# Performance work log

Measured on AMD Instinct MI355X. Metric: run time of the kernel, lower is better.

Reference implementation:

```python
import jax, jax.numpy as jnp
import numpy as np

NUM_EXPERTS = 8
TOP_K = 2
HIDDEN = 2048
INTER = 2048
SWIGLU_LIMIT = 7.0
BATCH, SEQ = 4, 2048


def setup_inputs() -> dict:
    key = jax.random.key(0)
    k0, k1, k2, k3, k4 = jax.random.split(key, 5)
    x = jax.random.normal(k0, (BATCH, SEQ, HIDDEN), jnp.float32)
    Wr = jax.random.normal(k1, (HIDDEN, NUM_EXPERTS), jnp.float32) * 0.02
    Wg = jax.random.normal(k2, (NUM_EXPERTS, HIDDEN, INTER), jnp.float32) * 0.02
    Wu = jax.random.normal(k3, (NUM_EXPERTS, HIDDEN, INTER), jnp.float32) * 0.02
    Wd = jax.random.normal(k4, (NUM_EXPERTS, INTER, HIDDEN), jnp.float32) * 0.02
    return {"hidden_states": x, "Wr": Wr, "Wg": Wg, "Wu": Wu, "Wd": Wd}


def reference(hidden_states, Wr, Wg, Wu, Wd):
    # Router: logits [B,S,E], top-k over experts, softmax over the k logits.
    router_logits = jnp.einsum('bsh,he->bse', hidden_states, Wr)
    topk_logits, selected = jax.lax.top_k(router_logits, TOP_K)  # [B,S,K]
    router_probs = jax.nn.softmax(topk_logits, axis=-1)          # [B,S,K]

    # Per-expert masked-dense SwiGLU. Because the Dense layers have no bias,
    # Expert(x * mask) == Expert(x) at selected positions and the combine
    # weight is 0 elsewhere, so running on unmasked x is mathematically
    # identical to the original's masked-input formulation.
    out = jnp.zeros_like(hidden_states)
    for e in range(NUM_EXPERTS):  # fixed structural loop over experts
        w_e = jnp.where(selected == e, router_probs, 0.0).sum(axis=-1, keepdims=True)  # [B,S,1]
        g = jnp.einsum('bsh,hi->bsi', hidden_states, Wg[e])
        g = jnp.clip(jax.nn.silu(g), -SWIGLU_LIMIT, SWIGLU_LIMIT)
        u = jnp.einsum('bsh,hi->bsi', hidden_states, Wu[e])
        h = jnp.einsum('bsi,ih->bsh', g * u, Wd[e])
        out = out + h * w_e
    return out
```

## Files before the change

### kernel.cpp

```cpp
#include <hip/hip_runtime.h>

#define TOKENS 8192
#define HID 2048
#define NEXP 8
#define NT 32

typedef float f32x4 __attribute__((ext_vector_type(4)));
typedef short bf16x8 __attribute__((ext_vector_type(8)));

#define WS_XBF     0ULL
#define WS_ACT     33554432ULL
#define WS_WCAT    100663296ULL
#define WS_WDT     234881024ULL
#define WS_ROWTOK  301989888ULL
#define WS_ROWPROB 302055424ULL
#define WS_EIDX    302120960ULL
#define WS_PROBS   302186496ULL
#define WS_META    302252032ULL

__device__ __forceinline__ unsigned short f2bf(float f) {
    union { float f; unsigned int u; } a; a.f = f;
    unsigned int r = a.u + 0x7fffu + ((a.u >> 16) & 1u);
    return (unsigned short)(r >> 16);
}

__device__ __forceinline__ void gload16(void* ldsdst, const void* gsrc) {
    __builtin_amdgcn_global_load_lds(
        (const __attribute__((address_space(1))) void*)gsrc,
        (__attribute__((address_space(3))) void*)ldsdst, 16, 0, 0);
}

#define BAR asm volatile("s_barrier" ::: "memory")
#define VM4 asm volatile("s_waitcnt vmcnt(4)" ::: "memory")
#define VM0 asm volatile("s_waitcnt vmcnt(0)" ::: "memory")

__global__ __launch_bounds__(256) void router_kernel(
    const float* __restrict__ x, const float* __restrict__ Wr,
    unsigned short* __restrict__ xbf, int2* __restrict__ eidx,
    float2* __restrict__ probs, int* __restrict__ meta) {
    __shared__ float wrt[NEXP * HID];
    int tid = threadIdx.x;
    for (int f = tid; f < HID * NEXP; f += 256) {
        int i = f >> 3, e = f & 7;
        wrt[e * HID + i] = Wr[f];
    }
    __syncthreads();
    int w = tid >> 6, l = tid & 63;
    int tok = blockIdx.x * 4 + w;
    const float4* xr = (const float4*)(x + (size_t)tok * HID);
    float acc[NEXP];
#pragma unroll
    for (int e = 0; e < NEXP; ++e) acc[e] = 0.f;
    unsigned long long* xbr = (unsigned long long*)(xbf + (size_t)tok * HID);
#pragma unroll
    for (int it = 0; it < 8; ++it) {
        float4 v = xr[it * 64 + l];
        int k0 = (it * 64 + l) * 4;
#pragma unroll
        for (int e = 0; e < NEXP; ++e) {
            float4 wv = *(const float4*)&wrt[e * HID + k0];
            acc[e] += v.x * wv.x + v.y * wv.y + v.z * wv.z + v.w * wv.w;
        }
        unsigned long long pk = (unsigned long long)f2bf(v.x)
                              | ((unsigned long long)f2bf(v.y) << 16)
                              | ((unsigned long long)f2bf(v.z) << 32)
                              | ((unsigned long long)f2bf(v.w) << 48);
        int qi = ((k0 >> 5) << 3) + (((k0 >> 2) & 3) << 1) + ((k0 >> 4) & 1);
        xbr[qi] = pk;
    }
#pragma unroll
    for (int e = 0; e < NEXP; ++e) {
#pragma unroll
        for (int d = 1; d < 64; d <<= 1) acc[e] += __shfl_xor(acc[e], d, 64);
    }
    if (l == 0) {
        int e0 = 0; float v0 = acc[0];
#pragma unroll
        for (int e = 1; e < NEXP; ++e) if (acc[e] > v0) { v0 = acc[e]; e0 = e; }
        int e1 = -1; float v1 = 0.f;
#pragma unroll
        for (int e = 0; e < NEXP; ++e)
            if (e != e0 && (e1 < 0 || acc[e] > v1)) { v1 = acc[e]; e1 = e; }
        float a = __expf(v1 - v0);
        float inv = 1.f / (1.f + a);
        int2 ei; ei.x = e0; ei.y = e1;
        float2 pp; pp.x = inv; pp.y = a * inv;
        eidx[tok] = ei;
        probs[tok] = pp;
        atomicAdd(&meta[e0], 1);
        atomicAdd(&meta[e1], 1);
    }
}

__global__ __launch_bounds__(256) void convert_kernel(
    const float* __restrict__ Wg, const float* __restrict__ Wu,
    const float* __restrict__ Wd, unsigned short* __restrict__ wcat,
    unsigned short* __restrict__ wdt) {
    int mz = blockIdx.z;
    int mat = mz >> 3, e = mz & 7;
    const float* W = (mat == 0 ? Wg : (mat == 1 ? Wu : Wd)) + (size_t)e * HID * HID;
    int kb = blockIdx.y * 64, nb = blockIdx.x * 64;
    __shared__ unsigned short t[64][68];
    int tid = threadIdx.x;
    int kr = tid >> 4;
    int nc = (tid & 15) * 4;
#pragma unroll
    for (int ki = 0; ki < 4; ++ki) {
        int k = kr + ki * 16;
        float4 v = *(const float4*)&W[(size_t)(kb + k) * HID + nb + nc];
        t[nc + 0][k] = f2bf(v.x);
        t[nc + 1][k] = f2bf(v.y);
        t[nc + 2][k] = f2bf(v.z);
        t[nc + 3][k] = f2bf(v.w);
    }
    __syncthreads();
    int q = tid & 15;
    int k0 = ((q >> 3) << 5) + (((q >> 1) & 3) << 2) + ((q & 1) << 4);
#pragma unroll
    for (int ni = 0; ni < 4; ++ni) {
        int n = (tid >> 4) + ni * 16;
        int gn = nb + n;
        unsigned short* orow;
        if (mat < 2)
            orow = wcat + ((size_t)e * 4096 + (gn >> 4) * 32 + mat * 16 + (gn & 15)) * HID;
        else
            orow = wdt + ((size_t)e * HID + gn) * HID;
        unsigned long long pk = (unsigned long long)t[n][k0]
                              | ((unsigned long long)t[n][k0 + 1] << 16)
                              | ((unsigned long long)t[n][k0 + 2] << 32)
                              | ((unsigned long long)t[n][k0 + 3] << 48);
        *(unsigned long long*)&orow[kb + q * 4] = pk;
    }
}

__global__ void scan_kernel(int* __restrict__ meta) {
    if (threadIdx.x == 0) {
        int s = 0;
#pragma unroll
        for (int e = 0; e < NEXP; ++e) { meta[16 + e] = s; s += meta[e]; }
    }
}

__global__ __launch_bounds__(256) void build_kernel(
    const int2* __restrict__ eidx, const float2* __restrict__ probs,
    int* __restrict__ meta, int* __restrict__ row_token, float* __restrict__ row_prob) {
    int t = blockIdx.x * 256 + threadIdx.x;
    if (t >= TOKENS) return;
    int2 e = eidx[t];
    float2 p = probs[t];
    int s0 = meta[16 + e.x] + atomicAdd(&meta[8 + e.x], 1);
    row_token[s0] = t; row_prob[s0] = p.x;
    int s1 = meta[16 + e.y] + atomicAdd(&meta[8 + e.y], 1);
    row_token[s1] = t; row_prob[s1] = p.y;
}

#define STA(dn, kh, tt) { char* _d = lds + (dn)*32768 + (kh)*16384 + tid*16; \
    gload16(_d,        a0 + (tt)*64 + (kh)*32); \
    gload16(_d + 8192, a1 + (tt)*64 + (kh)*32); }
#define STB(dn, kh, tt) { char* _d = lds + (dn)*32768 + 65536 + (kh)*16384 + tid*16; \
    gload16(_d,        b0 + (tt)*64 + (kh)*32); \
    gload16(_d + 8192, b1 + (tt)*64 + (kh)*32); }
#define LDA_TO(dst, d, kh) { const char* _b = lds + (d)*32768 + (kh)*16384 + afo; \
    dst[0] = *(const bf16x8*)(_b);        dst[1] = *(const bf16x8*)(_b + 1024); \
    dst[2] = *(const bf16x8*)(_b + 2048); dst[3] = *(const bf16x8*)(_b + 3072); \
    dst[4] = *(const bf16x8*)(_b + 4096); dst[5] = *(const bf16x8*)(_b + 5120); \
    dst[6] = *(const bf16x8*)(_b + 6144); dst[7] = *(const bf16x8*)(_b + 7168); }
#define LDB(d, kh, nn) (*(const bf16x8*)(lds + (d)*32768 + (kh)*16384 + bfo + (nn)*1024))
#define MM(A, B0, B1, n0, n1) do { \
    __builtin_amdgcn_s_setprio(1); \
    _Pragma("unroll") \
    for (int m = 0; m < 8; ++m) { \
        acc[m][n0] = __builtin_amdgcn_mfma_f32_16x16x32_bf16(A[m], B0, acc[m][n0], 0, 0, 0); \
        acc[m][n1] = __builtin_amdgcn_mfma_f32_16x16x32_bf16(A[m], B1, acc[m][n1], 0, 0, 0); \
    } \
    __builtin_amdgcn_s_setprio(0); \
} while (0)

#define GEMM_MAIN_LOOP \
    bf16x8 af[8], af2[8], bq0, bq1, bq2, bq3; \
    STA(0, 0, 0); STB(0, 0, 0); STA(0, 1, 0); STB(0, 1, 0); \
    VM4; BAR; \
    LDA_TO(af, 0, 0); bq0 = LDB(0, 0, 0); bq1 = LDB(0, 0, 1); \
    for (int t = 0; t < NT - 1; ++t) { \
        const int d = t & 1, dn = d ^ 1, tn = t + 1; \
        bq2 = LDB(d, 0, 2); bq3 = LDB(d, 0, 3); \
        STA(dn, 0, tn); \
        MM(af, bq0, bq1, 0, 1); \
        STB(dn, 0, tn); \
        VM4; BAR; \
        LDA_TO(af2, d, 1); bq0 = LDB(d, 1, 0); bq1 = LDB(d, 1, 1); \
        MM(af, bq2, bq3, 2, 3); \
        bq2 = LDB(d, 1, 2); bq3 = LDB(d, 1, 3); \
        STA(dn, 1, tn); \
        MM(af2, bq0, bq1, 0, 1); \
        STB(dn, 1, tn); \
        VM4; BAR; \
        LDA_TO(af, dn, 0); bq0 = LDB(dn, 0, 0); bq1 = LDB(dn, 0, 1); \
        MM(af2, bq2, bq3, 2, 3); \
    } \
    { const int d = (NT - 1) & 1; \
        bq2 = LDB(d, 0, 2); bq3 = LDB(d, 0, 3); \
        MM(af, bq0, bq1, 0, 1); \
        VM0; BAR; \
        LDA_TO(af2, d, 1); bq0 = LDB(d, 1, 0); bq1 = LDB(d, 1, 1); \
        MM(af, bq2, bq3, 2, 3); \
        bq2 = LDB(d, 1, 2); bq3 = LDB(d, 1, 3); \
        MM(af2, bq0, bq1, 0, 1); \
        MM(af2, bq2, bq3, 2, 3); \
    }

__global__ __launch_bounds__(512) void gemm1_kernel(
    const unsigned short* __restrict__ xbf, const unsigned short* __restrict__ wcat,
    const int* __restrict__ row_token, const int* __restrict__ meta,
    unsigned short* __restrict__ act) {
    int e = blockIdx.z;
    int cnt = meta[e];
    int rt = blockIdx.y;
    if (rt * 256 >= cnt) return;
    int off = meta[16 + e];
    int ct = blockIdx.x;
    __shared__ __align__(16) char lds[131072];
    int tid = threadIdx.x, w = tid >> 6, l = tid & 63;
    int wr = w >> 2, wc = w & 3;
    int r16 = l & 15, g = l >> 4;

    int srow = tid >> 2;
    int sxu = (tid & 3) ^ ((tid >> 3) & 3);
    int rr0 = rt * 256 + srow;       if (rr0 >= cnt) rr0 = cnt - 1;
    int rr1 = rt * 256 + srow + 128; if (rr1 >= cnt) rr1 = cnt - 1;
    const unsigned short* a0 = xbf + (size_t)row_token[off + rr0] * HID + sxu * 8;
    const unsigned short* a1 = xbf + (size_t)row_token[off + rr1] * HID + sxu * 8;
    const unsigned short* b0 = wcat + ((size_t)(e * 4096 + ct * 256 + srow)) * HID + sxu * 8;
    const unsigned short* b1 = b0 + (size_t)128 * HID;

    int sw = (r16 >> 1) & 3;
    int afo = (wr * 128 + r16) * 64 + (g ^ sw) * 16;
    int bfo = 65536 + (wc * 64 + r16) * 64 + (g ^ sw) * 16;

    f32x4 acc[8][4];
    f32x4 z = {0.f, 0.f, 0.f, 0.f};
#pragma unroll
    for (int m = 0; m < 8; ++m)
#pragma unroll
        for (int nn = 0; nn < 4; ++nn) acc[m][nn] = z;

    GEMM_MAIN_LOOP

    int pb = (ct * 4 + wc) * 32 + (r16 >> 2) * 8 + (r16 & 3);
#pragma unroll
    for (int m = 0; m < 8; ++m) {
        int rbase = wr * 128 + m * 16 + (l >> 4) * 4;
#pragma unroll
        for (int q = 0; q < 4; ++q) {
            int r = rt * 256 + rbase + q;
            if (r < cnt) {
                unsigned short* arow = act + (size_t)(off + r) * HID;
#pragma unroll
                for (int p = 0; p < 2; ++p) {
                    float gg = acc[m][2 * p][q];
                    float uu = acc[m][2 * p + 1][q];
                    float s = gg / (1.f + __expf(-gg));
                    s = fminf(fmaxf(s, -7.f), 7.f);
                    arow[pb + p * 4] = f2bf(s * uu);
                }
            }
        }
    }
}

__global__ __launch_bounds__(512) void gemm2_kernel(
    const unsigned short* __restrict__ act, const unsigned short* __restrict__ wdt,
    const int* __restrict__ row_token, const float* __restrict__ row_prob,
    const int* __restrict__ meta, float* __restrict__ out) {
    int e = blockIdx.z;
    int cnt = meta[e];
    int rt = blockIdx.y;
    if (rt * 256 >= cnt) return;
    int off = meta[16 + e];
    int ct = blockIdx.x;
    __shared__ __align__(16) char lds[131072];
    int tid = threadIdx.x, w = tid >> 6, l = tid & 63;
    int wr = w >> 2, wc = w & 3;
    int r16 = l & 15, g = l >> 4;

    int srow = tid >> 2;
    int sxu = (tid & 3) ^ ((tid >> 3) & 3);
    int rr0 = rt * 256 + srow;       if (rr0 >= cnt) rr0 = cnt - 1;
    int rr1 = rt * 256 + srow + 128; if (rr1 >= cnt) rr1 = cnt - 1;
    const unsigned short* a0 = act + (size_t)(off + rr0) * HID + sxu * 8;
    const unsigned short* a1 = act + (size_t)(off + rr1) * HID + sxu * 8;
    const unsigned short* b0 = wdt + ((size_t)(e * HID + ct * 256 + srow)) * HID + sxu * 8;
    const unsigned short* b1 = b0 + (size_t)128 * HID;

    int sw = (r16 >> 1) & 3;
    int afo = (wr * 128 + r16) * 64 + (g ^ sw) * 16;
    int bfo = 65536 + (wc * 64 + r16) * 64 + (g ^ sw) * 16;

    f32x4 acc[8][4];
    f32x4 z = {0.f, 0.f, 0.f, 0.f};
#pragma unroll
    for (int m = 0; m < 8; ++m)
#pragma unroll
        for (int nn = 0; nn < 4; ++nn) acc[m][nn] = z;

    GEMM_MAIN_LOOP

    int colb = ct * 256 + wc * 64;
#pragma unroll
    for (int m = 0; m < 8; ++m) {
        int rbase = wr * 128 + m * 16 + (l >> 4) * 4;
#pragma unroll
        for (int q = 0; q < 4; ++q) {
            int r = rt * 256 + rbase + q;
            if (r < cnt) {
                int slot = off + r;
                int tok = row_token[slot];
                float pr = row_prob[slot];
                float* orow = out + (size_t)tok * HID + colb;
#pragma unroll
                for (int nn = 0; nn < 4; ++nn)
                    unsafeAtomicAdd(&orow[nn * 16 + r16], acc[m][nn][q] * pr);
            }
        }
    }
}

extern "C" void kernel_launch(void* const* d_in, const int* in_sizes, int n_in,
                              void* d_out, int out_size, void* d_ws, size_t ws_size,
                              hipStream_t stream) {
    const float* x  = (const float*)d_in[0];
    const float* Wr = (const float*)d_in[1];
    const float* Wg = (const float*)d_in[2];
    const float* Wu = (const float*)d_in[3];
    const float* Wd = (const float*)d_in[4];
    float* out = (float*)d_out;
    char* ws = (char*)d_ws;

    unsigned short* xbf  = (unsigned short*)(ws + WS_XBF);
    unsigned short* act  = (unsigned short*)(ws + WS_ACT);
    unsigned short* wcat = (unsigned short*)(ws + WS_WCAT);
    unsigned short* wdt  = (unsigned short*)(ws + WS_WDT);
    int* row_token  = (int*)(ws + WS_ROWTOK);
    float* row_prob = (float*)(ws + WS_ROWPROB);
    int2* eidx      = (int2*)(ws + WS_EIDX);
    float2* probs   = (float2*)(ws + WS_PROBS);
    int* meta       = (int*)(ws + WS_META);

    hipMemsetAsync(d_out, 0, (size_t)out_size * sizeof(float), stream);
    hipMemsetAsync(meta, 0, 64, stream);

    hipLaunchKernelGGL(convert_kernel, dim3(32, 32, 24), dim3(256), 0, stream,
                       Wg, Wu, Wd, wcat, wdt);
    hipLaunchKernelGGL(router_kernel, dim3(TOKENS / 4), dim3(256), 0, stream,
                       x, Wr, xbf, eidx, probs, meta);
    hipLaunchKernelGGL(scan_kernel, dim3(1), dim3(64), 0, stream, meta);
    hipLaunchKernelGGL(build_kernel, dim3(TOKENS / 256), dim3(256), 0, stream,
                       eidx, probs, meta, row_token, row_prob);
    hipLaunchKernelGGL(gemm1_kernel, dim3(16, 64, NEXP), dim3(512), 0, stream,
                       xbf, wcat, row_token, meta, act);
    hipLaunchKernelGGL(gemm2_kernel, dim3(8, 64, NEXP), dim3(512), 0, stream,
                       act, wdt, row_token, row_prob, meta, out);
}
```

Baseline: 910.8 us.

## Restructure GEMM main loop into 4x4 MFMA sub-tiles with barriers; vectorize weight transpose stores

The GEMM main loop no longer prefetches A and B fragments from LDS across MMA phases. Each K-half is now split into two 4x4 MFMA sub-blocks: four A fragments and four B fragments are loaded, the code waits on lgkmcnt(0), then 16 MFMAs issue, with extra barriers between phases. This cuts fragment register use (afr[4] and bq[4] replace af[8], af2[8] and four bq registers), but it adds barriers and removes the overlap of LDS reads with MFMA. The weight prep kernel now has each thread write 32 contiguous bytes of a transposed row instead of 8-byte scattered stores.

```diff
diff --git a/kernel.cpp b/kernel.cpp
--- a/kernel.cpp
+++ b/kernel.cpp
@@ -30,9 +30,10 @@
         (__attribute__((address_space(3))) void*)ldsdst, 16, 0, 0);
 }
 
-#define BAR asm volatile("s_barrier" ::: "memory")
-#define VM4 asm volatile("s_waitcnt vmcnt(4)" ::: "memory")
-#define VM0 asm volatile("s_waitcnt vmcnt(0)" ::: "memory")
+#define BAR   asm volatile("s_barrier" ::: "memory")
+#define VM4   asm volatile("s_waitcnt vmcnt(4)" ::: "memory")
+#define VM0   asm volatile("s_waitcnt vmcnt(0)" ::: "memory")
+#define LGKM0 asm volatile("s_waitcnt lgkmcnt(0)" ::: "memory")
 
 __global__ __launch_bounds__(256) void router_kernel(
     const float* __restrict__ x, const float* __restrict__ Wr,
@@ -114,23 +115,23 @@
         t[nc + 3][k] = f2bf(v.w);
     }
     __syncthreads();
-    int q = tid & 15;
-    int k0 = ((q >> 3) << 5) + (((q >> 1) & 3) << 2) + ((q & 1) << 4);
-#pragma unroll
-    for (int ni = 0; ni < 4; ++ni) {
-        int n = (tid >> 4) + ni * 16;
-        int gn = nb + n;
-        unsigned short* orow;
-        if (mat < 2)
-            orow = wcat + ((size_t)e * 4096 + (gn >> 4) * 32 + mat * 16 + (gn & 15)) * HID;
-        else
-            orow = wdt + ((size_t)e * HID + gn) * HID;
-        unsigned long long pk = (unsigned long long)t[n][k0]
-                              | ((unsigned long long)t[n][k0 + 1] << 16)
-                              | ((unsigned long long)t[n][k0 + 2] << 32)
-                              | ((unsigned long long)t[n][k0 + 3] << 48);
-        *(unsigned long long*)&orow[kb + q * 4] = pk;
-    }
+    int n = tid >> 2;
+    int seg = tid & 3;
+    int gn = nb + n;
+    unsigned short* orow;
+    if (mat < 2)
+        orow = wcat + ((size_t)e * 4096 + (gn >> 4) * 32 + mat * 16 + (gn & 15)) * HID;
+    else
+        orow = wdt + ((size_t)e * HID + gn) * HID;
+    unsigned long long pk[4];
+#pragma unroll
+    for (int j = 0; j < 4; ++j) {
+        int qi = seg * 4 + j;
+        int klocal = ((qi >> 3) << 5) + (((qi >> 1) & 3) << 2) + ((qi & 1) << 4);
+        pk[j] = *(const unsigned long long*)&t[n][klocal];
+    }
+    unsigned long long* dst = (unsigned long long*)&orow[kb + seg * 16];
+    dst[0] = pk[0]; dst[1] = pk[1]; dst[2] = pk[2]; dst[3] = pk[3];
 }
 
 __global__ void scan_kernel(int* __restrict__ meta) {
@@ -160,53 +161,43 @@
 #define STB(dn, kh, tt) { char* _d = lds + (dn)*32768 + 65536 + (kh)*16384 + tid*16; \
     gload16(_d,        b0 + (tt)*64 + (kh)*32); \
     gload16(_d + 8192, b1 + (tt)*64 + (kh)*32); }
-#define LDA_TO(dst, d, kh) { const char* _b = lds + (d)*32768 + (kh)*16384 + afo; \
-    dst[0] = *(const bf16x8*)(_b);        dst[1] = *(const bf16x8*)(_b + 1024); \
-    dst[2] = *(const bf16x8*)(_b + 2048); dst[3] = *(const bf16x8*)(_b + 3072); \
-    dst[4] = *(const bf16x8*)(_b + 4096); dst[5] = *(const bf16x8*)(_b + 5120); \
-    dst[6] = *(const bf16x8*)(_b + 6144); dst[7] = *(const bf16x8*)(_b + 7168); }
-#define LDB(d, kh, nn) (*(const bf16x8*)(lds + (d)*32768 + (kh)*16384 + bfo + (nn)*1024))
-#define MM(A, B0, B1, n0, n1) do { \
+#define LDA4(d, kh, mb) { const char* _b = lds + (d)*32768 + (kh)*16384 + afo + (mb)*4096; \
+    afr[0] = *(const bf16x8*)(_b);        afr[1] = *(const bf16x8*)(_b + 1024); \
+    afr[2] = *(const bf16x8*)(_b + 2048); afr[3] = *(const bf16x8*)(_b + 3072); }
+#define LDB4(d, kh) { const char* _b = lds + (d)*32768 + (kh)*16384 + bfo; \
+    bq[0] = *(const bf16x8*)(_b);        bq[1] = *(const bf16x8*)(_b + 1024); \
+    bq[2] = *(const bf16x8*)(_b + 2048); bq[3] = *(const bf16x8*)(_b + 3072); }
+#define MM16(mb) do { \
     __builtin_amdgcn_s_setprio(1); \
     _Pragma("unroll") \
-    for (int m = 0; m < 8; ++m) { \
-        acc[m][n0] = __builtin_amdgcn_mfma_f32_16x16x32_bf16(A[m], B0, acc[m][n0], 0, 0, 0); \
-        acc[m][n1] = __builtin_amdgcn_mfma_f32_16x16x32_bf16(A[m], B1, acc[m][n1], 0, 0, 0); \
+    for (int _m = 0; _m < 4; ++_m) { \
+        _Pragma("unroll") \
+        for (int _n = 0; _n < 4; ++_n) \
+            acc[(mb)*4+_m][_n] = __builtin_amdgcn_mfma_f32_16x16x32_bf16(afr[_m], bq[_n], acc[(mb)*4+_m][_n], 0, 0, 0); \
     } \
     __builtin_amdgcn_s_setprio(0); \
 } while (0)
 
 #define GEMM_MAIN_LOOP \
-    bf16x8 af[8], af2[8], bq0, bq1, bq2, bq3; \
-    STA(0, 0, 0); STB(0, 0, 0); STA(0, 1, 0); STB(0, 1, 0); \
+    f32x4 acc[8][4]; \
+    { f32x4 z = {0.f,0.f,0.f,0.f}; \
+      _Pragma("unroll") for (int m=0;m<8;++m) \
+      _Pragma("unroll") for (int n=0;n<4;++n) acc[m][n]=z; } \
+    bf16x8 afr[4], bq[4]; \
+    STA(0,0,0); STB(0,0,0); STA(0,1,0); STB(0,1,0); \
     VM4; BAR; \
-    LDA_TO(af, 0, 0); bq0 = LDB(0, 0, 0); bq1 = LDB(0, 0, 1); \
     for (int t = 0; t < NT - 1; ++t) { \
         const int d = t & 1, dn = d ^ 1, tn = t + 1; \
-        bq2 = LDB(d, 0, 2); bq3 = LDB(d, 0, 3); \
-        STA(dn, 0, tn); \
-        MM(af, bq0, bq1, 0, 1); \
-        STB(dn, 0, tn); \
-        VM4; BAR; \
-        LDA_TO(af2, d, 1); bq0 = LDB(d, 1, 0); bq1 = LDB(d, 1, 1); \
-        MM(af, bq2, bq3, 2, 3); \
-        bq2 = LDB(d, 1, 2); bq3 = LDB(d, 1, 3); \
-        STA(dn, 1, tn); \
-        MM(af2, bq0, bq1, 0, 1); \
-        STB(dn, 1, tn); \
-        VM4; BAR; \
-        LDA_TO(af, dn, 0); bq0 = LDB(dn, 0, 0); bq1 = LDB(dn, 0, 1); \
-        MM(af2, bq2, bq3, 2, 3); \
+        LDB4(d,0); LDA4(d,0,0); STA(dn,0,tn); BAR; LGKM0; MM16(0); BAR; \
+        LDA4(d,0,1);            STB(dn,0,tn); BAR; LGKM0; MM16(1); VM4; BAR; \
+        LDB4(d,1); LDA4(d,1,0); STA(dn,1,tn); BAR; LGKM0; MM16(0); BAR; \
+        LDA4(d,1,1);            STB(dn,1,tn); BAR; LGKM0; MM16(1); VM4; BAR; \
     } \
     { const int d = (NT - 1) & 1; \
-        bq2 = LDB(d, 0, 2); bq3 = LDB(d, 0, 3); \
-        MM(af, bq0, bq1, 0, 1); \
-        VM0; BAR; \
-        LDA_TO(af2, d, 1); bq0 = LDB(d, 1, 0); bq1 = LDB(d, 1, 1); \
-        MM(af, bq2, bq3, 2, 3); \
-        bq2 = LDB(d, 1, 2); bq3 = LDB(d, 1, 3); \
-        MM(af2, bq0, bq1, 0, 1); \
-        MM(af2, bq2, bq3, 2, 3); \
+        LDB4(d,0); LDA4(d,0,0); BAR; LGKM0; MM16(0); BAR; \
+        LDA4(d,0,1);            BAR; LGKM0; MM16(1); VM0; BAR; \
+        LDB4(d,1); LDA4(d,1,0); BAR; LGKM0; MM16(0); BAR; \
+        LDA4(d,1,1);            LGKM0; MM16(1); \
     }
 
 __global__ __launch_bounds__(512) void gemm1_kernel(
@@ -222,7 +213,7 @@
     __shared__ __align__(16) char lds[131072];
     int tid = threadIdx.x, w = tid >> 6, l = tid & 63;
     int wr = w >> 2, wc = w & 3;
-    int r16 = l & 15, g = l >> 4;
+    int r16 = l & 15;
 
     int srow = tid >> 2;
     int sxu = (tid & 3) ^ ((tid >> 3) & 3);
@@ -234,15 +225,9 @@
     const unsigned short* b1 = b0 + (size_t)128 * HID;
 
     int sw = (r16 >> 1) & 3;
+    int g = l >> 4;
     int afo = (wr * 128 + r16) * 64 + (g ^ sw) * 16;
     int bfo = 65536 + (wc * 64 + r16) * 64 + (g ^ sw) * 16;
-
-    f32x4 acc[8][4];
-    f32x4 z = {0.f, 0.f, 0.f, 0.f};
-#pragma unroll
-    for (int m = 0; m < 8; ++m)
-#pragma unroll
-        for (int nn = 0; nn < 4; ++nn) acc[m][nn] = z;
 
     GEMM_MAIN_LOOP
 
@@ -281,7 +266,7 @@
     __shared__ __align__(16) char lds[131072];
     int tid = threadIdx.x, w = tid >> 6, l = tid & 63;
     int wr = w >> 2, wc = w & 3;
-    int r16 = l & 15, g = l >> 4;
+    int r16 = l & 15;
 
     int srow = tid >> 2;
     int sxu = (tid & 3) ^ ((tid >> 3) & 3);
@@ -293,15 +278,9 @@
     const unsigned short* b1 = b0 + (size_t)128 * HID;
 
     int sw = (r16 >> 1) & 3;
+    int g = l >> 4;
     int afo = (wr * 128 + r16) * 64 + (g ^ sw) * 16;
     int bfo = 65536 + (wc * 64 + r16) * 64 + (g ^ sw) * 16;
-
-    f32x4 acc[8][4];
-    f32x4 z = {0.f, 0.f, 0.f, 0.f};
-#pragma unroll
-    for (int m = 0; m < 8; ++m)
-#pragma unroll
-        for (int nn = 0; nn < 4; ++nn) acc[m][nn] = z;
 
     GEMM_MAIN_LOOP
 
```

After: 923.2 us (median of 2 runs). About the same (+1.4%).

## Compact expert row-tile list to skip empty GEMM blocks; widen weight-convert stores

Applied to the files above, without the earlier changes.

The scan kernel now builds a compact list of (expert, row-tile) pairs, capped at MAXTILES, and records how many there are. Both GEMM kernels launch a 2D grid over that list instead of a 3D grid padded to 64 tiles per expert. This removes thousands of blocks that would only exit early, at the cost of one extra indirection through meta. Separately, the weight-convert kernel now has each thread write 32 contiguous bytes of a row instead of scattered 8-byte stores, to improve write coalescing.

```diff
diff --git a/kernel.cpp b/kernel.cpp
--- a/kernel.cpp
+++ b/kernel.cpp
@@ -4,6 +4,7 @@
 #define HID 2048
 #define NEXP 8
 #define NT 32
+#define MAXTILES 72
 
 typedef float f32x4 __attribute__((ext_vector_type(4)));
 typedef short bf16x8 __attribute__((ext_vector_type(8)));
@@ -114,30 +115,38 @@
         t[nc + 3][k] = f2bf(v.w);
     }
     __syncthreads();
-    int q = tid & 15;
-    int k0 = ((q >> 3) << 5) + (((q >> 1) & 3) << 2) + ((q & 1) << 4);
-#pragma unroll
-    for (int ni = 0; ni < 4; ++ni) {
-        int n = (tid >> 4) + ni * 16;
-        int gn = nb + n;
-        unsigned short* orow;
-        if (mat < 2)
-            orow = wcat + ((size_t)e * 4096 + (gn >> 4) * 32 + mat * 16 + (gn & 15)) * HID;
-        else
-            orow = wdt + ((size_t)e * HID + gn) * HID;
-        unsigned long long pk = (unsigned long long)t[n][k0]
-                              | ((unsigned long long)t[n][k0 + 1] << 16)
-                              | ((unsigned long long)t[n][k0 + 2] << 32)
-                              | ((unsigned long long)t[n][k0 + 3] << 48);
-        *(unsigned long long*)&orow[kb + q * 4] = pk;
-    }
+    int n = tid >> 2;
+    int seg = tid & 3;
+    int gn = nb + n;
+    unsigned short* orow;
+    if (mat < 2)
+        orow = wcat + ((size_t)e * 4096 + (gn >> 4) * 32 + mat * 16 + (gn & 15)) * HID;
+    else
+        orow = wdt + ((size_t)e * HID + gn) * HID;
+    unsigned long long pk[4];
+#pragma unroll
+    for (int j = 0; j < 4; ++j) {
+        int qi = seg * 4 + j;
+        int klocal = ((qi >> 3) << 5) + (((qi >> 1) & 3) << 2) + ((qi & 1) << 4);
+        pk[j] = *(const unsigned long long*)&t[n][klocal];
+    }
+    unsigned long long* dst = (unsigned long long*)&orow[kb + seg * 16];
+    dst[0] = pk[0]; dst[1] = pk[1]; dst[2] = pk[2]; dst[3] = pk[3];
 }
 
 __global__ void scan_kernel(int* __restrict__ meta) {
     if (threadIdx.x == 0) {
-        int s = 0;
-#pragma unroll
-        for (int e = 0; e < NEXP; ++e) { meta[16 + e] = s; s += meta[e]; }
+        int s = 0, tiles = 0;
+#pragma unroll
+        for (int e = 0; e < NEXP; ++e) {
+            meta[16 + e] = s;
+            int c = meta[e];
+            int nt = (c + 255) >> 8;
+            for (int i = 0; i < nt && tiles < MAXTILES; ++i)
+                meta[32 + tiles++] = (e << 8) | i;
+            s += c;
+        }
+        meta[24] = tiles;
     }
 }
 
@@ -177,6 +186,10 @@
 } while (0)
 
 #define GEMM_MAIN_LOOP \
+    f32x4 acc[8][4]; \
+    { f32x4 z = {0.f,0.f,0.f,0.f}; \
+      _Pragma("unroll") for (int m=0;m<8;++m) \
+      _Pragma("unroll") for (int n=0;n<4;++n) acc[m][n]=z; } \
     bf16x8 af[8], af2[8], bq0, bq1, bq2, bq3; \
     STA(0, 0, 0); STB(0, 0, 0); STA(0, 1, 0); STB(0, 1, 0); \
     VM4; BAR; \
@@ -213,10 +226,11 @@
     const unsigned short* __restrict__ xbf, const unsigned short* __restrict__ wcat,
     const int* __restrict__ row_token, const int* __restrict__ meta,
     unsigned short* __restrict__ act) {
-    int e = blockIdx.z;
+    int ty = blockIdx.y;
+    if (ty >= meta[24]) return;
+    int mp = meta[32 + ty];
+    int e = mp >> 8, rt = mp & 255;
     int cnt = meta[e];
-    int rt = blockIdx.y;
-    if (rt * 256 >= cnt) return;
     int off = meta[16 + e];
     int ct = blockIdx.x;
     __shared__ __align__(16) char lds[131072];
@@ -236,13 +250,6 @@
     int sw = (r16 >> 1) & 3;
     int afo = (wr * 128 + r16) * 64 + (g ^ sw) * 16;
     int bfo = 65536 + (wc * 64 + r16) * 64 + (g ^ sw) * 16;
-
-    f32x4 acc[8][4];
-    f32x4 z = {0.f, 0.f, 0.f, 0.f};
-#pragma unroll
-    for (int m = 0; m < 8; ++m)
-#pragma unroll
-        for (int nn = 0; nn < 4; ++nn) acc[m][nn] = z;
 
     GEMM_MAIN_LOOP
 
@@ -272,10 +279,11 @@
     const unsigned short* __restrict__ act, const unsigned short* __restrict__ wdt,
     const int* __restrict__ row_token, const float* __restrict__ row_prob,
     const int* __restrict__ meta, float* __restrict__ out) {
-    int e = blockIdx.z;
+    int ty = blockIdx.y;
+    if (ty >= meta[24]) return;
+    int mp = meta[32 + ty];
+    int e = mp >> 8, rt = mp & 255;
     int cnt = meta[e];
-    int rt = blockIdx.y;
-    if (rt * 256 >= cnt) return;
     int off = meta[16 + e];
     int ct = blockIdx.x;
     __shared__ __align__(16) char lds[131072];
@@ -295,13 +303,6 @@
     int sw = (r16 >> 1) & 3;
     int afo = (wr * 128 + r16) * 64 + (g ^ sw) * 16;
     int bfo = 65536 + (wc * 64 + r16) * 64 + (g ^ sw) * 16;
-
-    f32x4 acc[8][4];
-    f32x4 z = {0.f, 0.f, 0.f, 0.f};
-#pragma unroll
-    for (int m = 0; m < 8; ++m)
-#pragma unroll
-        for (int nn = 0; nn < 4; ++nn) acc[m][nn] = z;
 
     GEMM_MAIN_LOOP
 
@@ -356,8 +357,8 @@
     hipLaunchKernelGGL(scan_kernel, dim3(1), dim3(64), 0, stream, meta);
     hipLaunchKernelGGL(build_kernel, dim3(TOKENS / 256), dim3(256), 0, stream,
                        eidx, probs, meta, row_token, row_prob);
-    hipLaunchKernelGGL(gemm1_kernel, dim3(16, 64, NEXP), dim3(512), 0, stream,
+    hipLaunchKernelGGL(gemm1_kernel, dim3(16, MAXTILES), dim3(512), 0, stream,
                        xbf, wcat, row_token, meta, act);
-    hipLaunchKernelGGL(gemm2_kernel, dim3(8, 64, NEXP), dim3(512), 0, stream,
+    hipLaunchKernelGGL(gemm2_kernel, dim3(8, MAXTILES), dim3(512), 0, stream,
                        act, wdt, row_token, row_prob, meta, out);
 }
```

Result: no change. 915.5 us (median of 2 runs) (+0.5%).
